# Optimization experiments

Measured on AMD Instinct MI355X. Metric: run time of the kernel, lower is better.

Reference implementation:

```python
import jax, jax.numpy as jnp
import numpy as np

B, T, C, H, N, FFN = 4, 1024, 2048, 32, 64, 7168
HEAD_DIVISOR = 8.0
EPS = 1e-5


def setup_inputs() -> dict:
    key = jax.random.key(0)
    ks = jax.random.split(key, 30)
    rn = lambda k, s, sc=0.02: jax.random.normal(k, s, jnp.float32) * sc
    ru = lambda k, s: jax.random.uniform(k, s, jnp.float32)
    return {
        "x": jax.random.normal(ks[0], (B, T, C), jnp.float32),
        "att_shift": jax.random.normal(ks[1], (B, C), jnp.float32),
        "wkv_state": jax.random.normal(ks[2], (B, H, N, N), jnp.float32) * 0.1,
        "ffn_shift": jax.random.normal(ks[3], (B, C), jnp.float32),
        "ln1_w": jnp.ones((C,), jnp.float32), "ln1_b": jnp.zeros((C,), jnp.float32),
        "ln2_w": jnp.ones((C,), jnp.float32), "ln2_b": jnp.zeros((C,), jnp.float32),
        "mix_k": ru(ks[4], (C,)), "mix_v": ru(ks[5], (C,)),
        "mix_r": ru(ks[6], (C,)), "mix_g": ru(ks[7], (C,)),
        "Wr": rn(ks[8], (C, C)), "Wk": rn(ks[9], (C, C)), "Wv": rn(ks[10], (C, C)),
        "Wg": rn(ks[11], (C, C)), "Wo": rn(ks[12], (C, C)),
        "time_decay": jax.random.normal(ks[13], (H, N), jnp.float32) * 0.5,
        "time_faaaa": jax.random.normal(ks[14], (H, N), jnp.float32) * 0.1,
        "gn_w": jnp.ones((C,), jnp.float32), "gn_b": jnp.zeros((C,), jnp.float32),
        "cmix_k": ru(ks[15], (C,)), "cmix_r": ru(ks[16], (C,)),
        "Wck": rn(ks[17], (C, FFN)), "Wcr": rn(ks[18], (C, C)), "Wcv": rn(ks[19], (FFN, C)),
    }


def _ln(z, w, b):
    m = z.mean(-1, keepdims=True)
    v = z.var(-1, keepdims=True)
    return (z - m) / jnp.sqrt(v + EPS) * w + b


def _shift(x, shift_state):
    # prepend carried last-token state, drop final position
    return jnp.concatenate([shift_state[:, None, :], x[:, :-1]], axis=1)


def reference(x, att_shift, wkv_state, ffn_shift, ln1_w, ln1_b, ln2_w, ln2_b,
              mix_k, mix_v, mix_r, mix_g, Wr, Wk, Wv, Wg, Wo,
              time_decay, time_faaaa, gn_w, gn_b, cmix_k, cmix_r, Wck, Wcr, Wcv):
    Bb, Tt, Cc = x.shape

    # ---- TimeMix ----
    x1 = _ln(x, ln1_w, ln1_b)
    xx = _shift(x1, att_shift)
    xk = x1 * mix_k + xx * (1 - mix_k)
    xv = x1 * mix_v + xx * (1 - mix_v)
    xr = x1 * mix_r + xx * (1 - mix_r)
    xg = x1 * mix_g + xx * (1 - mix_g)
    r = (xr @ Wr).reshape(Bb, Tt, H, N)
    k = (xk @ Wk).reshape(Bb, Tt, H, N)
    v = (xv @ Wv).reshape(Bb, Tt, H, N)
    g = jax.nn.silu(xg @ Wg)

    w = jnp.exp(-jnp.exp(time_decay))[None, :, :, None]  # [1,H,N,1] decay on k-index
    u = time_faaaa[None, :, :, None]                      # [1,H,N,1] bonus on current token

    def step(S, rkv):  # S: [B,H,N,N] (k-index i, v-index j)
        rr, kk, vv = rkv
        kv = kk[..., :, None] * vv[..., None, :]          # [B,H,N,N]
        y = jnp.einsum('bhi,bhij->bhj', rr, S + u * kv)
        return S * w + kv, y

    rkv = (jnp.moveaxis(r, 1, 0), jnp.moveaxis(k, 1, 0), jnp.moveaxis(v, 1, 0))
    new_wkv, ys = jax.lax.scan(step, wkv_state, rkv)      # ys: [T,B,H,N]
    att = jnp.moveaxis(ys, 0, 1)                          # [B,T,H,N]

    # GroupNorm(n_head groups) on att / head_size_divisor
    z = att / HEAD_DIVISOR
    m = z.mean(-1, keepdims=True)
    var = z.var(-1, keepdims=True)
    z = (z - m) / jnp.sqrt(var + EPS)
    z = z * gn_w.reshape(H, N) + gn_b.reshape(H, N)
    att_out = (z.reshape(Bb, Tt, Cc) * g) @ Wo

    x = x + att_out

    # ---- ChannelMix ----
    x2 = _ln(x, ln2_w, ln2_b)
    xx2 = _shift(x2, ffn_shift)
    xck = x2 * cmix_k + xx2 * (1 - cmix_k)
    xcr = x2 * cmix_r + xx2 * (1 - cmix_r)
    kk = jnp.square(jax.nn.relu(xck @ Wck))
    kv = kk @ Wcv
    ffn_out = jax.nn.sigmoid(xcr @ Wcr) * kv
    x = x + ffn_out

    return x, x1[:, -1], new_wkv, x2[:, -1]
```

## Files before the change

### kernel.cpp

```cpp
#include <hip/hip_runtime.h>
#include <cstdint>
#include <cstddef>

typedef unsigned short u16;
typedef unsigned int u32;
typedef short bf16x8 __attribute__((ext_vector_type(8)));
typedef unsigned short u16x4 __attribute__((ext_vector_type(4)));
typedef unsigned short u16x8 __attribute__((ext_vector_type(8)));
typedef float f32x4 __attribute__((ext_vector_type(4)));

#define DEV __device__ __forceinline__

constexpr int Bb = 4, Tt = 1024, Cc = 2048, Hh = 32, Nd = 64, FF = 7168;
constexpr int BT = Bb * Tt;
constexpr int NCH = 16;

DEV u16 f2bf(float f) {
  union { float f; unsigned u; } un; un.f = f;
  unsigned r = un.u + 0x7FFFu + ((un.u >> 16) & 1u);
  return (u16)(r >> 16);
}
DEV float bf2f(u16 h) {
  union { unsigned u; float f; } un; un.u = ((unsigned)h) << 16;
  return un.f;
}
DEV void gll16(const u16* gp, u16* lp) {
  __builtin_amdgcn_global_load_lds(
      (const __attribute__((address_space(1))) unsigned int*)gp,
      (__attribute__((address_space(3))) unsigned int*)lp,
      16, 0, 0);
}
DEV int xcd_swz(int f, int nwg) {
  int q = nwg >> 3;
  return (f & 7) * q + (f >> 3);
}

DEV void transp_body(const float* __restrict__ W, u16* __restrict__ Wt,
                     int Kk, int Nn, float (*tile)[33]) {
  int n0 = blockIdx.x * 32, k0 = blockIdx.y * 32;
  int tx = threadIdx.x & 31, ty = threadIdx.x >> 5;
  #pragma unroll
  for (int r = 0; r < 32; r += 8)
    tile[r + ty][tx] = W[(size_t)(k0 + r + ty) * Nn + n0 + tx];
  __syncthreads();
  #pragma unroll
  for (int r = 0; r < 32; r += 8)
    Wt[(size_t)(n0 + r + ty) * Kk + k0 + tx] = f2bf(tile[tx][r + ty]);
}

__global__ void transpose_to_bf16(const float* __restrict__ W, u16* __restrict__ Wt,
                                  int Kk, int Nn) {
  __shared__ float tile[32][33];
  transp_body(W, Wt, Kk, Nn, tile);
}

__global__ void transpose6_cc(const float* __restrict__ W0, const float* __restrict__ W1,
                              const float* __restrict__ W2, const float* __restrict__ W3,
                              const float* __restrict__ W4, const float* __restrict__ W5,
                              u16* __restrict__ T0, u16* __restrict__ T1,
                              u16* __restrict__ T2, u16* __restrict__ T3,
                              u16* __restrict__ T4, u16* __restrict__ T5) {
  __shared__ float tile[32][33];
  const int z = blockIdx.z;
  const float* W = (z == 0) ? W0 : (z == 1) ? W1 : (z == 2) ? W2 :
                   (z == 3) ? W3 : (z == 4) ? W4 : W5;
  u16* T = (z == 0) ? T0 : (z == 1) ? T1 : (z == 2) ? T2 :
           (z == 3) ? T3 : (z == 4) ? T4 : T5;
  transp_body(W, T, Cc, Cc, tile);
}

DEV void block_ln(const float* __restrict__ src, int tid, float* red,
                  float vals[8], float& mean, float& inv) {
  float s = 0.f, ss = 0.f;
  #pragma unroll
  for (int i = 0; i < 8; i++) {
    float t = src[tid + i * 256];
    vals[i] = t; s += t; ss += t * t;
  }
  #pragma unroll
  for (int m = 1; m < 64; m <<= 1) { s += __shfl_xor(s, m); ss += __shfl_xor(ss, m); }
  int lane = tid & 63, wv = tid >> 6;
  __syncthreads();
  if (lane == 0) { red[wv] = s; red[4 + wv] = ss; }
  __syncthreads();
  s = red[0] + red[1] + red[2] + red[3];
  ss = red[4] + red[5] + red[6] + red[7];
  mean = s * (1.f / Cc);
  float var = ss * (1.f / Cc) - mean * mean;
  inv = rsqrtf(var + 1e-5f);
}

__global__ __launch_bounds__(256)
void ln_mix4(const float* __restrict__ x, const float* __restrict__ shift,
             const float* __restrict__ w, const float* __restrict__ b,
             const float* __restrict__ mk, const float* __restrict__ mv,
             const float* __restrict__ mr, const float* __restrict__ mg,
             u16* __restrict__ xk, u16* __restrict__ xv,
             u16* __restrict__ xr, u16* __restrict__ xg,
             float* __restrict__ last) {
  int row = blockIdx.x;
  int t = row & (Tt - 1), bb = row >> 10;
  int tid = threadIdx.x;
  __shared__ float red[8];
  const float* cur = x + (size_t)row * Cc;
  float cv[8], pv[8], cm, ci, pm = 0.f, pi = 1.f;
  block_ln(cur, tid, red, cv, cm, ci);
  bool t0 = (t == 0);
  const float* prev = t0 ? (shift + (size_t)bb * Cc) : (cur - Cc);
  if (!t0) {
    block_ln(prev, tid, red, pv, pm, pi);
  } else {
    #pragma unroll
    for (int i = 0; i < 8; i++) pv[i] = prev[tid + i * 256];
  }
  size_t o = (size_t)row * Cc;
  bool isLast = (t == Tt - 1);
  #pragma unroll
  for (int i = 0; i < 8; i++) {
    int c = tid + i * 256;
    float xc = (cv[i] - cm) * ci * w[c] + b[c];
    float xp = t0 ? pv[i] : (pv[i] - pm) * pi * w[c] + b[c];
    xk[o + c] = f2bf(xp + mk[c] * (xc - xp));
    xv[o + c] = f2bf(xp + mv[c] * (xc - xp));
    xr[o + c] = f2bf(xp + mr[c] * (xc - xp));
    xg[o + c] = f2bf(xp + mg[c] * (xc - xp));
    if (isLast) last[(size_t)bb * Cc + c] = xc;
  }
}

__global__ __launch_bounds__(256)
void ln_mix2(const float* __restrict__ x, const float* __restrict__ shift,
             const float* __restrict__ w, const float* __restrict__ b,
             const float* __restrict__ ck, const float* __restrict__ cr,
             u16* __restrict__ xck, u16* __restrict__ xcr,
             float* __restrict__ last) {
  int row = blockIdx.x;
  int t = row & (Tt - 1), bb = row >> 10;
  int tid = threadIdx.x;
  __shared__ float red[8];
  const float* cur = x + (size_t)row * Cc;
  float cv[8], pv[8], cm, ci, pm = 0.f, pi = 1.f;
  block_ln(cur, tid, red, cv, cm, ci);
  bool t0 = (t == 0);
  const float* prev = t0 ? (shift + (size_t)bb * Cc) : (cur - Cc);
  if (!t0) {
    block_ln(prev, tid, red, pv, pm, pi);
  } else {
    #pragma unroll
    for (int i = 0; i < 8; i++) pv[i] = prev[tid + i * 256];
  }
  size_t o = (size_t)row * Cc;
  bool isLast = (t == Tt - 1);
  #pragma unroll
  for (int i = 0; i < 8; i++) {
    int c = tid + i * 256;
    float xc = (cv[i] - cm) * ci * w[c] + b[c];
    float xp = t0 ? pv[i] : (pv[i] - pm) * pi * w[c] + b[c];
    xck[o + c] = f2bf(xp + ck[c] * (xc - xp));
    xcr[o + c] = f2bf(xp + cr[c] * (xc - xp));
    if (isLast) last[(size_t)bb * Cc + c] = xc;
  }
}

DEV int swzoff(int row, int off) {
  return (row << 7) +
         (off ^ ((((row >> 1) & 1) << 4) | (((row >> 2) & 1) << 5) | (((row >> 3) & 1) << 6)));
}

DEV void stage_half(const u16* __restrict__ gbase, int ldK, u16* slot, int tid) {
  #pragma unroll
  for (int c2 = 0; c2 < 2; c2++) {
    const int D = c2 * 8192 + tid * 16;
    const int row = D >> 7;
    const int off = (D & 127) ^ ((((row >> 1) & 1) << 4) | (((row >> 2) & 1) << 5) | (((row >> 3) & 1) << 6));
    gll16(gbase + (size_t)row * ldK + (off >> 1), (u16*)((char*)slot + D));
  }
}

template <int EPI, int NB>
DEV void g256_core(const u16* __restrict__ A, const u16* __restrict__ Bt,
                   int N, int K, int ldK,
                   float* __restrict__ Co, u16* __restrict__ Cb,
                   const float* __restrict__ X1, const float* __restrict__ X2,
                   const u16* __restrict__ X2b,
                   u16 (*lds)[8192], int m0, int n0, int act) {
  const int tid = threadIdx.x;
  const int w = tid >> 6, lane = tid & 63;
  const int l15 = lane & 15, l4 = lane >> 4;
  const int wm = (w & 3) * 64;
  const int wn = (w >> 2) * (NB * 64);
  const int ahalf = wm >> 7;
  const int arow0 = wm & 127;
  const int bhalf = (NB == 2) ? (w >> 2) : 0;
  const int nt = K >> 6;

  const u16* Ag = A + (size_t)m0 * ldK;
  const u16* Bg = Bt + (size_t)n0 * ldK;

  f32x4 acc[4][NB * 4] = {};
  bf16x8 a[4][2];

  stage_half(Ag, ldK, lds[0], tid);
  stage_half(Ag + (size_t)128 * ldK, ldK, lds[1], tid);
  stage_half(Bg, ldK, lds[4], tid);
  if constexpr (NB == 2) stage_half(Bg + (size_t)128 * ldK, ldK, lds[5], tid);
  if (nt > 1) {
    stage_half(Ag + 64, ldK, lds[2], tid);
    stage_half(Ag + (size_t)128 * ldK + 64, ldK, lds[3], tid);
    asm volatile("s_waitcnt vmcnt(4)" ::: "memory");
  } else {
    asm volatile("s_waitcnt vmcnt(0)" ::: "memory");
  }
  asm volatile("s_barrier" ::: "memory");

  for (int t = 0; t < nt; t++) {
    const int buf = t & 1;
    const char* Aslot = (const char*)lds[buf * 2 + ahalf];
    const char* Bslot = (const char*)lds[4 + buf * NB + bhalf];

#define G256_PHASE(p)                                                                       \
    {                                                                                       \
      constexpr int nh = (p) >> 1, kh = (p) & 1;                                            \
      if constexpr ((p) < 2) {                                                              \
        _Pragma("unroll")                                                                   \
        for (int mf = 0; mf < 4; mf++) {                                                    \
          const int row = arow0 + mf * 16 + l15;                                            \
          a[mf][kh] = *(const bf16x8*)(Aslot + swzoff(row, kh * 64 + l4 * 16));             \
        }                                                                                   \
      }                                                                                     \
      bf16x8 bfr[2 * NB];                                                                   \
      _Pragma("unroll")                                                                     \
      for (int j = 0; j < 2 * NB; j++) {                                                    \
        const int row = (NB == 2 ? 0 : wn) + (nh * 2 * NB + j) * 16 + l15;                  \
        bfr[j] = *(const bf16x8*)(Bslot + swzoff(row, kh * 64 + l4 * 16));                  \
      }                                                                                     \
      if constexpr ((p) == 0) {                                                             \
        if (t + 1 < nt) stage_half(Bg + (size_t)(t + 1) * 64, ldK,                          \
                                   lds[4 + ((t + 1) & 1) * NB], tid);                       \
      } else if constexpr ((p) == 1) {                                                      \
        if constexpr (NB == 2) {                                                            \
          if (t + 1 < nt) stage_half(Bg + (size_t)128 * ldK + (size_t)(t + 1) * 64, ldK,    \
                                     lds[4 + ((t + 1) & 1) * NB + 1], tid);                 \
        }                                                                                   \
      } else if constexpr ((p) == 2) {                                                      \
        if (t + 2 < nt) stage_half(Ag + (size_t)(t + 2) * 64, ldK, lds[buf << 1], tid);     \
      } else {                                                                              \
        if (t + 2 < nt) stage_half(Ag + (size_t)128 * ldK + (size_t)(t + 2) * 64, ldK,      \
                                   lds[(buf << 1) + 1], tid);                               \
      }                                                                                     \
      asm volatile("s_barrier" ::: "memory");                                               \
      __builtin_amdgcn_s_setprio(1);                                                       \
      _Pragma("unroll")                                                                     \
      for (int mf = 0; mf < 4; mf++)                                                        \
        _Pragma("unroll")                                                                   \
        for (int j = 0; j < 2 * NB; j++)                                                    \
          acc[mf][nh * 2 * NB + j] = __builtin_amdgcn_mfma_f32_16x16x32_bf16(               \
              a[mf][kh], bfr[j], acc[mf][nh * 2 * NB + j], 0, 0, 0);                        \
      __builtin_amdgcn_s_setprio(0);                                                       \
      if constexpr ((p) == 3) {                                                             \
        if (t + 2 < nt) asm volatile("s_waitcnt vmcnt(4)" ::: "memory");                    \
        else            asm volatile("s_waitcnt vmcnt(0)" ::: "memory");                    \
      }                                                                                     \
      asm volatile("s_barrier" ::: "memory");                                               \
    }

    G256_PHASE(0)
    G256_PHASE(1)
    G256_PHASE(2)
    G256_PHASE(3)
#undef G256_PHASE
  }

  #pragma unroll
  for (int mf = 0; mf < 4; mf++) {
    #pragma unroll
    for (int reg = 0; reg < 4; reg++) {
      const int gr = m0 + wm + mf * 16 + l4 * 4 + reg;
      const size_t ro = (size_t)gr * N;
      #pragma unroll
      for (int nf = 0; nf < NB * 4; nf++) {
        const int gc = n0 + wn + nf * 16 + l15;
        float val = acc[mf][nf][reg];
        if constexpr (EPI == 0) {
          Co[ro + gc] = val;
        } else if constexpr (EPI == 1) {
          if (act) val = val / (1.f + __expf(-val));
          Cb[ro + gc] = f2bf(val);
        } else if constexpr (EPI == 3) {
          float tr = fmaxf(val, 0.f);
          Cb[ro + gc] = f2bf(tr * tr);
        } else if constexpr (EPI == 4) {
          Co[ro + gc] = X1[ro + gc] + val;
        } else {
          float s = 1.f / (1.f + __expf(-val));
          float kvv = X2[ro + gc] + bf2f(X2b[ro + gc]);
          Co[ro + gc] = fmaf(s, kvv, X1[ro + gc]);
        }
      }
    }
  }
}

template <int EPI>
__global__ __launch_bounds__(512)
void gemm256s(const u16* __restrict__ A, const u16* __restrict__ Bt,
              int N, int K,
              float* __restrict__ Co, u16* __restrict__ Cb,
              const float* __restrict__ X1, int NX) {
  __shared__ __align__(16) u16 lds[8][8192];
  int o = xcd_swz(blockIdx.x, gridDim.x);
  int xb = o % NX, yb = o / NX;
  g256_core<EPI, 2>(A, Bt, N, K, K, Co, Cb, X1, nullptr, nullptr, lds,
                    yb * 256, xb * 256, 0);
}

template <int EPI>
__global__ __launch_bounds__(512)
void gemm128s(const u16* __restrict__ A, const u16* __restrict__ Bt,
              int N, int K,
              float* __restrict__ Co, u16* __restrict__ Cb,
              const float* __restrict__ X1, const float* __restrict__ X2,
              const u16* __restrict__ X2b, int NX) {
  __shared__ __align__(16) u16 lds[6][8192];
  int o = xcd_swz(blockIdx.x, gridDim.x);
  int xb = o % NX, yb = o / NX;
  g256_core<EPI, 1>(A, Bt, N, K, K, Co, Cb, X1, X2, X2b, lds,
                    yb * 256, xb * 128, 0);
}

__global__ __launch_bounds__(512)
void gemm256_proj(const u16* __restrict__ A0, const u16* __restrict__ A1,
                  const u16* __restrict__ A2, const u16* __restrict__ A3,
                  const u16* __restrict__ B0, const u16* __restrict__ B1,
                  const u16* __restrict__ B2, const u16* __restrict__ B3,
                  u16* __restrict__ C0, u16* __restrict__ C1,
                  u16* __restrict__ C2, u16* __restrict__ C3) {
  __shared__ __align__(16) u16 lds[8][8192];
  int o = xcd_swz(blockIdx.x, gridDim.x);
  int xb = o & 7, yb = (o >> 3) & 15, z = o >> 7;
  const u16* A = (z == 0) ? A0 : (z == 1) ? A1 : (z == 2) ? A2 : A3;
  const u16* Bt = (z == 0) ? B0 : (z == 1) ? B1 : (z == 2) ? B2 : B3;
  u16* Cb = (z == 0) ? C0 : (z == 1) ? C1 : (z == 2) ? C2 : C3;
  g256_core<1, 2>(A, Bt, Cc, Cc, Cc, nullptr, Cb, nullptr, nullptr, nullptr, lds,
                  yb * 256, xb * 256, z == 3);
}

__global__ __launch_bounds__(512)
void gemm256_splitk(const u16* __restrict__ A, const u16* __restrict__ Bt,
                    float* __restrict__ kv0, u16* __restrict__ kv1) {
  __shared__ __align__(16) u16 lds[8][8192];
  int o = xcd_swz(blockIdx.x, gridDim.x);
  int xb = o & 7, yb = (o >> 3) & 15, z = o >> 7;
  const int Koff = z * (FF / 2);
  if (z == 0)
    g256_core<0, 2>(A + Koff, Bt + Koff, Cc, FF / 2, FF, kv0, nullptr,
                    nullptr, nullptr, nullptr, lds, yb * 256, xb * 256, 0);
  else
    g256_core<1, 2>(A + Koff, Bt + Koff, Cc, FF / 2, FF, nullptr, kv1,
                    nullptr, nullptr, nullptr, lds, yb * 256, xb * 256, 0);
}

__global__ __launch_bounds__(256)
void wkv_pre(const u16* __restrict__ rg, const u16* __restrict__ kg,
             const u16* __restrict__ vg, const float* __restrict__ td,
             const float* __restrict__ tf,
             float* __restrict__ Yb, float* __restrict__ Db,
             u16* __restrict__ Rtb) {
  __shared__ float Pt[64][68];
  __shared__ float uL[64];
  __shared__ u16 rB[64 * 72];
  __shared__ u16 kB[64 * 72];
  __shared__ u16 Rh[64 * 72];
  __shared__ u16 KhX[96 * 72];
  __shared__ u16 vA[64 * 72];
  __shared__ u16 Vt[64 * 72];

  const int tid = threadIdx.x, bid = blockIdx.x;
  const int bh = bid >> 4, c = bid & 15;
  const int b = bh >> 5, h = bh & 31;
  const int lane = tid & 63, w = tid >> 6;

  {
    int i = tid & 63;
    float d = __expf(td[h * 64 + i]);
    float c1 = -1.4426950408889634f * d;
    int e0 = (tid >> 6) * 16;
    #pragma unroll
    for (int e = 0; e < 16; e++) Pt[e0 + e][i] = exp2f(c1 * (float)(e0 + e));
    if (tid < 64) uL[tid] = tf[h * 64 + tid];
  }
  __syncthreads();

  const int row = tid >> 2, col0 = (tid & 3) * 16;
  const int tl = row & 15;
  {
    size_t gro = ((size_t)b * Tt + c * 64 + row) * Cc + h * 64 + col0;
    u16x8 rv0 = *(const u16x8*)(rg + gro);
    u16x8 rv1 = *(const u16x8*)(rg + gro + 8);
    u16x8 kv0 = *(const u16x8*)(kg + gro);
    u16x8 kv1 = *(const u16x8*)(kg + gro + 8);
    u16x8 vv0 = *(const u16x8*)(vg + gro);
    u16x8 vv1 = *(const u16x8*)(vg + gro + 8);
    *(u16x8*)&rB[row * 72 + col0] = rv0; *(u16x8*)&rB[row * 72 + col0 + 8] = rv1;
    *(u16x8*)&kB[row * 72 + col0] = kv0; *(u16x8*)&kB[row * 72 + col0 + 8] = kv1;
    *(u16x8*)&vA[row * 72 + col0] = vv0; *(u16x8*)&vA[row * 72 + col0 + 8] = vv1;
    float rf[16], kf[16];
    #pragma unroll
    for (int e = 0; e < 8; e++) { rf[e] = bf2f(rv0[e]); rf[8 + e] = bf2f(rv1[e]); }
    #pragma unroll
    for (int e = 0; e < 8; e++) { kf[e] = bf2f(kv0[e]); kf[8 + e] = bf2f(kv1[e]); }
    u16x8 o0, o1, t0_, t1_;
    #pragma unroll
    for (int e = 0; e < 8; e++) {
      o0[e] = f2bf(rf[e] * Pt[tl][col0 + e]);
      o1[e] = f2bf(rf[8 + e] * Pt[tl][col0 + 8 + e]);
      t0_[e] = f2bf(rf[e] * Pt[row][col0 + e]);
      t1_[e] = f2bf(rf[8 + e] * Pt[row][col0 + 8 + e]);
    }
    *(u16x8*)&Rh[row * 72 + col0] = o0; *(u16x8*)&Rh[row * 72 + col0 + 8] = o1;
    u16* rtp = Rtb + (size_t)bid * 4096 + row * 64 + col0;
    *(u16x8*)rtp = t0_; *(u16x8*)(rtp + 8) = t1_;
    if (row < 48) {
      u16x8 a0, a1;
      #pragma unroll
      for (int e = 0; e < 8; e++) {
        a0[e] = f2bf(kf[e] * Pt[15 - tl][col0 + e]);
        a1[e] = f2bf(kf[8 + e] * Pt[15 - tl][col0 + 8 + e]);
      }
      *(u16x8*)&KhX[row * 72 + col0] = a0; *(u16x8*)&KhX[row * 72 + col0 + 8] = a1;
    }
    if (row < 32) {
      u16x8 a0, a1;
      #pragma unroll
      for (int e = 0; e < 8; e++) {
        a0[e] = f2bf(kf[e] * Pt[31 - tl][col0 + e]);
        a1[e] = f2bf(kf[8 + e] * Pt[31 - tl][col0 + 8 + e]);
      }
      *(u16x8*)&KhX[(48 + row) * 72 + col0] = a0; *(u16x8*)&KhX[(48 + row) * 72 + col0 + 8] = a1;
    }
    if (row < 16) {
      u16x8 a0, a1;
      #pragma unroll
      for (int e = 0; e < 8; e++) {
        a0[e] = f2bf(kf[e] * Pt[47 - tl][col0 + e]);
        a1[e] = f2bf(kf[8 + e] * Pt[47 - tl][col0 + 8 + e]);
      }
      *(u16x8*)&KhX[(80 + row) * 72 + col0] = a0; *(u16x8*)&KhX[(80 + row) * 72 + col0 + 8] = a1;
    }
  }
  __syncthreads();

  {
    const int jj = tid & 63, s0 = (tid >> 6) * 16;
    #pragma unroll
    for (int ds = 0; ds < 16; ds += 2) {
      u32 pk = ((u32)vA[(s0 + ds + 1) * 72 + jj] << 16) | vA[(s0 + ds) * 72 + jj];
      *(u32*)&Vt[jj * 72 + s0 + ds] = pk;
    }
  }
  __syncthreads();

  u16* aB = vA;
  {
    const int pr[6] = {1, 2, 3, 2, 3, 3};
    const int qr[6] = {0, 1, 2, 0, 1, 0};
    const int dr[6] = {0, 0, 0, 1, 1, 2};
    const int lr = lane & 15, kq = lane >> 4;
    for (int pi = w; pi < 6; pi += 4) {
      const int p = pr[pi], q = qr[pi], d = dr[pi];
      const int kbase = (d == 0) ? q * 16 : (d == 1) ? 48 + q * 16 : 80 + q * 16;
      f32x4 aacc = {};
      #pragma unroll
      for (int kf2 = 0; kf2 < 2; kf2++) {
        bf16x8 af = *(const bf16x8*)&Rh[(p * 16 + lr) * 72 + kf2 * 32 + kq * 8];
        bf16x8 bf_ = *(const bf16x8*)&KhX[(kbase + lr) * 72 + kf2 * 32 + kq * 8];
        aacc = __builtin_amdgcn_mfma_f32_16x16x32_bf16(af, bf_, aacc, 0, 0, 0);
      }
      #pragma unroll
      for (int reg = 0; reg < 4; reg++) {
        aB[(p * 16 + kq * 4 + reg) * 72 + q * 16 + lr] = f2bf(aacc[reg]);
        aB[(q * 16 + kq * 4 + reg) * 72 + p * 16 + lr] = 0;
      }
    }
    for (int e = lane; e < 256; e += 64) {
      const int tl2 = e >> 4, sl = e & 15;
      float a = 0.f;
      if (sl <= tl2) {
        const u16* rp = &rB[(w * 16 + tl2) * 72];
        const u16* kp = &kB[(w * 16 + sl) * 72];
        const float* pp = (sl == tl2) ? uL : &Pt[tl2 - 1 - sl][0];
        #pragma unroll
        for (int i0 = 0; i0 < 64; i0 += 4) {
          u16x4 ra = *(const u16x4*)(rp + i0);
          u16x4 ka = *(const u16x4*)(kp + i0);
          f32x4 pa = *(const f32x4*)(pp + i0);
          #pragma unroll
          for (int di = 0; di < 4; di++)
            a = fmaf(bf2f(ra[di]) * bf2f(ka[di]), pa[di], a);
        }
      }
      aB[(w * 16 + tl2) * 72 + w * 16 + sl] = f2bf(a);
    }
  }
  __syncthreads();

  u16* Ktt = KhX;
  {
    const int ii = tid & 63, s0 = (tid >> 6) * 16;
    #pragma unroll
    for (int ds = 0; ds < 16; ds += 2) {
      float v0 = bf2f(kB[(s0 + ds) * 72 + ii]) * Pt[63 - (s0 + ds)][ii];
      float v1 = bf2f(kB[(s0 + ds + 1) * 72 + ii]) * Pt[63 - (s0 + ds + 1)][ii];
      u32 pk = ((u32)f2bf(v1) << 16) | f2bf(v0);
      *(u32*)&Ktt[ii * 72 + s0 + ds] = pk;
    }
  }
  __syncthreads();

  const int lr = lane & 15, kq = lane >> 4;
  {
    f32x4 yac[4] = {};
    #pragma unroll
    for (int kf2 = 0; kf2 < 2; kf2++) {
      bf16x8 af = *(const bf16x8*)&aB[(w * 16 + lr) * 72 + kf2 * 32 + kq * 8];
      #pragma unroll
      for (int nf = 0; nf < 4; nf++) {
        bf16x8 bf_ = *(const bf16x8*)&Vt[(nf * 16 + lr) * 72 + kf2 * 32 + kq * 8];
        yac[nf] = __builtin_amdgcn_mfma_f32_16x16x32_bf16(af, bf_, yac[nf], 0, 0, 0);
      }
    }
    float* Yp = Yb + (size_t)bid * 4096;
    #pragma unroll
    for (int nf = 0; nf < 4; nf++)
      #pragma unroll
      for (int reg = 0; reg < 4; reg++)
        Yp[(w * 16 + kq * 4 + reg) * 64 + nf * 16 + lr] = yac[nf][reg];

    f32x4 dac[4] = {};
    #pragma unroll
    for (int kf2 = 0; kf2 < 2; kf2++) {
      bf16x8 af = *(const bf16x8*)&Ktt[(w * 16 + lr) * 72 + kf2 * 32 + kq * 8];
      #pragma unroll
      for (int nf = 0; nf < 4; nf++) {
        bf16x8 bf_ = *(const bf16x8*)&Vt[(nf * 16 + lr) * 72 + kf2 * 32 + kq * 8];
        dac[nf] = __builtin_amdgcn_mfma_f32_16x16x32_bf16(af, bf_, dac[nf], 0, 0, 0);
      }
    }
    float* Dp = Db + (size_t)bid * 4096;
    #pragma unroll
    for (int nf = 0; nf < 4; nf++)
      #pragma unroll
      for (int reg = 0; reg < 4; reg++)
        Dp[(w * 16 + kq * 4 + reg) * 64 + nf * 16 + lr] = dac[nf][reg];
  }
}

__global__ __launch_bounds__(256)
void wkv_scan(const float* __restrict__ s0g, const float* __restrict__ td,
              const float* __restrict__ Db, u16* __restrict__ Sbb,
              float* __restrict__ sout) {
  const int bh = blockIdx.x, h = bh & 31;
  const int tid = threadIdx.x;
  const int i = tid >> 2, j0 = (tid & 3) * 16;
  float d = __expf(td[h * 64 + i]);
  float w64 = exp2f(-1.4426950408889634f * d * 64.f);
  f32x4 S[4];
  const float* sp = s0g + ((size_t)bh * 64 + i) * 64 + j0;
  #pragma unroll
  for (int q = 0; q < 4; q++) S[q] = *(const f32x4*)(sp + q * 4);
  for (int c = 0; c < NCH; c++) {
    u16* op = Sbb + ((size_t)(bh * 16 + c)) * 4096 + i * 64 + j0;
    u16x8 o0, o1;
    #pragma unroll
    for (int e = 0; e < 4; e++) { o0[e] = f2bf(S[0][e]); o0[4 + e] = f2bf(S[1][e]);
                                  o1[e] = f2bf(S[2][e]); o1[4 + e] = f2bf(S[3][e]); }
    *(u16x8*)op = o0; *(u16x8*)(op + 8) = o1;
    const float* dp = Db + ((size_t)(bh * 16 + c)) * 4096 + i * 64 + j0;
    #pragma unroll
    for (int q = 0; q < 4; q++) {
      f32x4 dv = *(const f32x4*)(dp + q * 4);
      #pragma unroll
      for (int e = 0; e < 4; e++) S[q][e] = fmaf(w64, S[q][e], dv[e]);
    }
  }
  float* fo = sout + ((size_t)bh * 64 + i) * 64 + j0;
  #pragma unroll
  for (int q = 0; q < 4; q++) *(f32x4*)(fo + q * 4) = S[q];
}

__global__ __launch_bounds__(256)
void wkv_post(const u16* __restrict__ Rtb, const u16* __restrict__ Sbb,
              const float* __restrict__ Yb, const u16* __restrict__ g,
              const float* __restrict__ gnw, const float* __restrict__ gnb,
              u16* __restrict__ xo) {
  __shared__ u16 Rt[64 * 72];
  __shared__ u16 St[64 * 72];
  __shared__ u16 xoL[64 * 72];
  const int tid = threadIdx.x, bid = blockIdx.x;
  const int bh = bid >> 4, c = bid & 15;
  const int b = bh >> 5, h = bh & 31;
  const int lane = tid & 63, w = tid >> 6;
  const int row = tid >> 2, col0 = (tid & 3) * 16;

  {
    const u16* rp = Rtb + (size_t)bid * 4096 + row * 64 + col0;
    u16x8 a0 = *(const u16x8*)rp, a1 = *(const u16x8*)(rp + 8);
    *(u16x8*)&Rt[row * 72 + col0] = a0; *(u16x8*)&Rt[row * 72 + col0 + 8] = a1;
  }
  {
    const u16* sp = Sbb + ((size_t)(bh * 16 + c)) * 4096 + row * 64 + col0;
    u16x8 s0 = *(const u16x8*)sp, s1 = *(const u16x8*)(sp + 8);
    #pragma unroll
    for (int e = 0; e < 8; e++) {
      St[(col0 + e) * 72 + row] = s0[e];
      St[(col0 + 8 + e) * 72 + row] = s1[e];
    }
  }
  const int lr = lane & 15, kq = lane >> 4;
  f32x4 acc[4];
  {
    const float* Yp = Yb + (size_t)bid * 4096;
    #pragma unroll
    for (int nf = 0; nf < 4; nf++)
      #pragma unroll
      for (int reg = 0; reg < 4; reg++)
        acc[nf][reg] = Yp[(w * 16 + kq * 4 + reg) * 64 + nf * 16 + lr];
  }
  __syncthreads();
  #pragma unroll
  for (int kf2 = 0; kf2 < 2; kf2++) {
    bf16x8 af = *(const bf16x8*)&Rt[(w * 16 + lr) * 72 + kf2 * 32 + kq * 8];
    #pragma unroll
    for (int nf = 0; nf < 4; nf++) {
      bf16x8 bf_ = *(const bf16x8*)&St[(nf * 16 + lr) * 72 + kf2 * 32 + kq * 8];
      acc[nf] = __builtin_amdgcn_mfma_f32_16x16x32_bf16(af, bf_, acc[nf], 0, 0, 0);
    }
  }
  #pragma unroll
  for (int reg = 0; reg < 4; reg++) {
    float s = 0.f, ss = 0.f;
    #pragma unroll
    for (int nf = 0; nf < 4; nf++) {
      float z = acc[nf][reg] * 0.125f;
      s += z; ss += z * z;
    }
    #pragma unroll
    for (int m = 1; m < 16; m <<= 1) { s += __shfl_xor(s, m); ss += __shfl_xor(ss, m); }
    float mean = s * (1.f / 64.f);
    float var = ss * (1.f / 64.f) - mean * mean;
    float inv = rsqrtf(var + 1e-5f);
    const int tau = w * 16 + kq * 4 + reg;
    #pragma unroll
    for (int nf = 0; nf < 4; nf++) {
      const int col = nf * 16 + lr;
      float z = acc[nf][reg] * 0.125f;
      float zn = (z - mean) * inv * gnw[h * 64 + col] + gnb[h * 64 + col];
      float gv = bf2f(g[((size_t)b * Tt + c * 64 + tau) * Cc + h * 64 + col]);
      xoL[tau * 72 + col] = f2bf(zn * gv);
    }
  }
  __syncthreads();
  {
    u16x8 o0 = *(const u16x8*)&xoL[row * 72 + col0];
    u16x8 o1 = *(const u16x8*)&xoL[row * 72 + col0 + 8];
    u16* xop = xo + ((size_t)b * Tt + c * 64 + row) * Cc + h * 64 + col0;
    *(u16x8*)xop = o0; *(u16x8*)(xop + 8) = o1;
  }
}

extern "C" void kernel_launch(void* const* d_in, const int* in_sizes, int n_in,
                              void* d_out, int out_size, void* d_ws, size_t ws_size,
                              hipStream_t stream) {
  const float* x         = (const float*)d_in[0];
  const float* att_shift = (const float*)d_in[1];
  const float* wkv0      = (const float*)d_in[2];
  const float* ffn_shift = (const float*)d_in[3];
  const float* ln1w = (const float*)d_in[4];
  const float* ln1b = (const float*)d_in[5];
  const float* ln2w = (const float*)d_in[6];
  const float* ln2b = (const float*)d_in[7];
  const float* mixk = (const float*)d_in[8];
  const float* mixv = (const float*)d_in[9];
  const float* mixr = (const float*)d_in[10];
  const float* mixg = (const float*)d_in[11];
  const float* Wr = (const float*)d_in[12];
  const float* Wk = (const float*)d_in[13];
  const float* Wv = (const float*)d_in[14];
  const float* Wg = (const float*)d_in[15];
  const float* Wo = (const float*)d_in[16];
  const float* td = (const float*)d_in[17];
  const float* tf = (const float*)d_in[18];
  const float* gnw = (const float*)d_in[19];
  const float* gnb = (const float*)d_in[20];
  const float* cmk = (const float*)d_in[21];
  const float* cmr = (const float*)d_in[22];
  const float* Wck = (const float*)d_in[23];
  const float* Wcr = (const float*)d_in[24];
  const float* Wcv = (const float*)d_in[25];

  constexpr size_t SZ_CC = (size_t)Cc * Cc * 2;
  constexpr size_t SZ_CF = (size_t)Cc * FF * 2;
  constexpr size_t SZ_AB = (size_t)BT * Cc * 2;
  constexpr size_t O_W   = 0;
  constexpr size_t O_R1  = 6 * SZ_CC + 2 * SZ_CF;
  constexpr size_t R1_SZ = 4 * SZ_AB;
  constexpr size_t O_R2  = O_R1 + R1_SZ;
  constexpr size_t R2_SZ = 3 * SZ_AB;
  constexpr size_t O_R3  = O_R2 + R2_SZ;
  constexpr size_t WS_NEED = O_R3 + SZ_AB;

  if (ws_size < WS_NEED) return;

  char* ws = (char*)d_ws;
  u16* WrT  = (u16*)(ws + O_W);
  u16* WkT  = (u16*)(ws + O_W + 1 * SZ_CC);
  u16* WvT  = (u16*)(ws + O_W + 2 * SZ_CC);
  u16* WgT  = (u16*)(ws + O_W + 3 * SZ_CC);
  u16* WoT  = (u16*)(ws + O_W + 4 * SZ_CC);
  u16* WcrT = (u16*)(ws + O_W + 5 * SZ_CC);
  u16* WckT = (u16*)(ws + O_W + 6 * SZ_CC);
  u16* WcvT = (u16*)(ws + O_W + 6 * SZ_CC + SZ_CF);

  u16*   xk  = (u16*)(ws + O_R1);
  u16*   xv  = (u16*)(ws + O_R1 + SZ_AB);
  u16*   xr  = (u16*)(ws + O_R1 + 2 * SZ_AB);
  u16*   xg  = (u16*)(ws + O_R1 + 3 * SZ_AB);
  float* Yb  = (float*)(ws + O_R1);
  u16*   Rtb = (u16*)(ws + O_R1 + 2 * SZ_AB);
  u16*   Sbb = (u16*)(ws + O_R1 + 3 * SZ_AB);
  u16*   kk  = (u16*)(ws + O_R1);
  u16*   rb  = (u16*)(ws + O_R2);
  u16*   kb  = (u16*)(ws + O_R2 + SZ_AB);
  u16*   vb  = (u16*)(ws + O_R2 + 2 * SZ_AB);
  u16*   xcr = (u16*)(ws + O_R2);
  u16*   xck = (u16*)(ws + O_R2 + SZ_AB);
  u16*   xo  = (u16*)(ws + O_R2 + 2 * SZ_AB);
  float* kv0 = (float*)(ws + O_R2 + SZ_AB);
  u16*   gbuf = (u16*)(ws + O_R3);
  u16*   kv1  = (u16*)(ws + O_R3);

  float* out      = (float*)d_out;
  float* x1_last  = out + (size_t)BT * Cc;
  float* wkv_out  = x1_last + (size_t)Bb * Cc;
  float* x2_last  = wkv_out + (size_t)Bb * Hh * Nd * Nd;
  float* Db       = out;

  transpose6_cc<<<dim3(64, 64, 6), 256, 0, stream>>>(Wr, Wk, Wv, Wg, Wo, Wcr,
                                                     WrT, WkT, WvT, WgT, WoT, WcrT);
  transpose_to_bf16<<<dim3(224, 64), 256, 0, stream>>>(Wck, WckT, Cc, FF);
  transpose_to_bf16<<<dim3(64, 224), 256, 0, stream>>>(Wcv, WcvT, FF, Cc);

  ln_mix4<<<BT, 256, 0, stream>>>(x, att_shift, ln1w, ln1b,
                                  mixk, mixv, mixr, mixg, xk, xv, xr, xg, x1_last);
  gemm256_proj<<<512, 512, 0, stream>>>(xr, xk, xv, xg,
                                        WrT, WkT, WvT, WgT,
                                        rb, kb, vb, gbuf);
  wkv_pre<<<Bb * Hh * NCH, 256, 0, stream>>>(rb, kb, vb, td, tf, Yb, Db, Rtb);
  wkv_scan<<<Bb * Hh, 256, 0, stream>>>(wkv0, td, Db, Sbb, wkv_out);
  wkv_post<<<Bb * Hh * NCH, 256, 0, stream>>>(Rtb, Sbb, Yb, gbuf, gnw, gnb, xo);
  gemm128s<4><<<256, 512, 0, stream>>>(xo, WoT, Cc, Cc, out, nullptr, x,
                                       nullptr, nullptr, 16);
  ln_mix2<<<BT, 256, 0, stream>>>(out, ffn_shift, ln2w, ln2b, cmk, cmr, xck, xcr, x2_last);
  gemm256s<3><<<448, 512, 0, stream>>>(xck, WckT, FF, Cc, nullptr, kk, nullptr, 28);
  gemm256_splitk<<<256, 512, 0, stream>>>(kk, WcvT, kv0, kv1);
  gemm128s<6><<<256, 512, 0, stream>>>(xcr, WcrT, Cc, Cc, out, nullptr, out,
                                       kv0, kv1, 16);

  (void)in_sizes; (void)n_in; (void)out_size;
}
```

Before: 724.5 us.

## Switch 256-tile GEMM core to 32x32x16 MFMA and vectorize weight transposes

The shared 256-wide GEMM core moves from 16x16x32 bf16 MFMA to 32x32x16 MFMA. Its k-loop is restructured into two half-phases per K tile, with A fragments loaded once per tile and the epilogue row/column mapping rewritten for the 32x32 accumulator layout. The aim is fewer LDS fragment reads per FLOP and fewer MFMA issues. Separately, the fp32-to-bf16 weight transposes drop the LDS tile and instead use 4x4 register transposes with float4 loads and 8-byte stores. The transposes trade some coalescing on the strided bf16 writes for less LDS traffic and synchronization.

```diff
diff --git a/kernel.cpp b/kernel.cpp
--- a/kernel.cpp
+++ b/kernel.cpp
@@ -8,6 +8,7 @@
 typedef unsigned short u16x4 __attribute__((ext_vector_type(4)));
 typedef unsigned short u16x8 __attribute__((ext_vector_type(8)));
 typedef float f32x4 __attribute__((ext_vector_type(4)));
+typedef float f32x16 __attribute__((ext_vector_type(16)));
 
 #define DEV __device__ __forceinline__
 
@@ -35,38 +36,41 @@
   return (f & 7) * q + (f >> 3);
 }
 
-DEV void transp_body(const float* __restrict__ W, u16* __restrict__ Wt,
-                     int Kk, int Nn, float (*tile)[33]) {
-  int n0 = blockIdx.x * 32, k0 = blockIdx.y * 32;
-  int tx = threadIdx.x & 31, ty = threadIdx.x >> 5;
-  #pragma unroll
-  for (int r = 0; r < 32; r += 8)
-    tile[r + ty][tx] = W[(size_t)(k0 + r + ty) * Nn + n0 + tx];
-  __syncthreads();
-  #pragma unroll
-  for (int r = 0; r < 32; r += 8)
-    Wt[(size_t)(n0 + r + ty) * Kk + k0 + tx] = f2bf(tile[tx][r + ty]);
-}
-
-__global__ void transpose_to_bf16(const float* __restrict__ W, u16* __restrict__ Wt,
-                                  int Kk, int Nn) {
-  __shared__ float tile[32][33];
-  transp_body(W, Wt, Kk, Nn, tile);
-}
-
-__global__ void transpose6_cc(const float* __restrict__ W0, const float* __restrict__ W1,
-                              const float* __restrict__ W2, const float* __restrict__ W3,
-                              const float* __restrict__ W4, const float* __restrict__ W5,
-                              u16* __restrict__ T0, u16* __restrict__ T1,
-                              u16* __restrict__ T2, u16* __restrict__ T3,
-                              u16* __restrict__ T4, u16* __restrict__ T5) {
-  __shared__ float tile[32][33];
+DEV void transp64_body(const float* __restrict__ W, u16* __restrict__ Wt,
+                       int Kk, int Nn) {
+  const int n0 = blockIdx.x * 64, k0 = blockIdx.y * 64;
+  const int tx = threadIdx.x & 15, ty = threadIdx.x >> 4;
+  const int kk = k0 + ty * 4, nn = n0 + tx * 4;
+  const float* p = W + (size_t)kk * Nn + nn;
+  f32x4 r0 = *(const f32x4*)(p);
+  f32x4 r1 = *(const f32x4*)(p + (size_t)Nn);
+  f32x4 r2 = *(const f32x4*)(p + 2 * (size_t)Nn);
+  f32x4 r3 = *(const f32x4*)(p + 3 * (size_t)Nn);
+  #pragma unroll
+  for (int j = 0; j < 4; j++) {
+    u16x4 o;
+    o[0] = f2bf(r0[j]); o[1] = f2bf(r1[j]); o[2] = f2bf(r2[j]); o[3] = f2bf(r3[j]);
+    *(u16x4*)(Wt + (size_t)(nn + j) * Kk + kk) = o;
+  }
+}
+
+__global__ void transp64(const float* __restrict__ W, u16* __restrict__ Wt,
+                         int Kk, int Nn) {
+  transp64_body(W, Wt, Kk, Nn);
+}
+
+__global__ void transp64_6cc(const float* __restrict__ W0, const float* __restrict__ W1,
+                             const float* __restrict__ W2, const float* __restrict__ W3,
+                             const float* __restrict__ W4, const float* __restrict__ W5,
+                             u16* __restrict__ T0, u16* __restrict__ T1,
+                             u16* __restrict__ T2, u16* __restrict__ T3,
+                             u16* __restrict__ T4, u16* __restrict__ T5) {
   const int z = blockIdx.z;
   const float* W = (z == 0) ? W0 : (z == 1) ? W1 : (z == 2) ? W2 :
                    (z == 3) ? W3 : (z == 4) ? W4 : W5;
   u16* T = (z == 0) ? T0 : (z == 1) ? T1 : (z == 2) ? T2 :
            (z == 3) ? T3 : (z == 4) ? T4 : T5;
-  transp_body(W, T, Cc, Cc, tile);
+  transp64_body(W, T, Cc, Cc);
 }
 
 DEV void block_ln(const float* __restrict__ src, int tid, float* red,
@@ -186,7 +190,7 @@
                    u16 (*lds)[8192], int m0, int n0, int act) {
   const int tid = threadIdx.x;
   const int w = tid >> 6, lane = tid & 63;
-  const int l15 = lane & 15, l4 = lane >> 4;
+  const int l31 = lane & 31, l5 = lane >> 5;
   const int wm = (w & 3) * 64;
   const int wn = (w >> 2) * (NB * 64);
   const int ahalf = wm >> 7;
@@ -197,8 +201,8 @@
   const u16* Ag = A + (size_t)m0 * ldK;
   const u16* Bg = Bt + (size_t)n0 * ldK;
 
-  f32x4 acc[4][NB * 4] = {};
-  bf16x8 a[4][2];
+  f32x16 acc[2][2 * NB] = {};
+  bf16x8 a[2][4];
 
   stage_half(Ag, ldK, lds[0], tid);
   stage_half(Ag + (size_t)128 * ldK, ldK, lds[1], tid);
@@ -218,68 +222,77 @@
     const char* Aslot = (const char*)lds[buf * 2 + ahalf];
     const char* Bslot = (const char*)lds[4 + buf * NB + bhalf];
 
-#define G256_PHASE(p)                                                                       \
-    {                                                                                       \
-      constexpr int nh = (p) >> 1, kh = (p) & 1;                                            \
-      if constexpr ((p) < 2) {                                                              \
-        _Pragma("unroll")                                                                   \
-        for (int mf = 0; mf < 4; mf++) {                                                    \
-          const int row = arow0 + mf * 16 + l15;                                            \
-          a[mf][kh] = *(const bf16x8*)(Aslot + swzoff(row, kh * 64 + l4 * 16));             \
-        }                                                                                   \
-      }                                                                                     \
-      bf16x8 bfr[2 * NB];                                                                   \
-      _Pragma("unroll")                                                                     \
-      for (int j = 0; j < 2 * NB; j++) {                                                    \
-        const int row = (NB == 2 ? 0 : wn) + (nh * 2 * NB + j) * 16 + l15;                  \
-        bfr[j] = *(const bf16x8*)(Bslot + swzoff(row, kh * 64 + l4 * 16));                  \
-      }                                                                                     \
-      if constexpr ((p) == 0) {                                                             \
-        if (t + 1 < nt) stage_half(Bg + (size_t)(t + 1) * 64, ldK,                          \
-                                   lds[4 + ((t + 1) & 1) * NB], tid);                       \
-      } else if constexpr ((p) == 1) {                                                      \
-        if constexpr (NB == 2) {                                                            \
-          if (t + 1 < nt) stage_half(Bg + (size_t)128 * ldK + (size_t)(t + 1) * 64, ldK,    \
-                                     lds[4 + ((t + 1) & 1) * NB + 1], tid);                 \
-        }                                                                                   \
-      } else if constexpr ((p) == 2) {                                                      \
-        if (t + 2 < nt) stage_half(Ag + (size_t)(t + 2) * 64, ldK, lds[buf << 1], tid);     \
-      } else {                                                                              \
-        if (t + 2 < nt) stage_half(Ag + (size_t)128 * ldK + (size_t)(t + 2) * 64, ldK,      \
-                                   lds[(buf << 1) + 1], tid);                               \
-      }                                                                                     \
-      asm volatile("s_barrier" ::: "memory");                                               \
-      __builtin_amdgcn_s_setprio(1);                                                       \
-      _Pragma("unroll")                                                                     \
-      for (int mf = 0; mf < 4; mf++)                                                        \
-        _Pragma("unroll")                                                                   \
-        for (int j = 0; j < 2 * NB; j++)                                                    \
-          acc[mf][nh * 2 * NB + j] = __builtin_amdgcn_mfma_f32_16x16x32_bf16(               \
-              a[mf][kh], bfr[j], acc[mf][nh * 2 * NB + j], 0, 0, 0);                        \
-      __builtin_amdgcn_s_setprio(0);                                                       \
-      if constexpr ((p) == 3) {                                                             \
-        if (t + 2 < nt) asm volatile("s_waitcnt vmcnt(4)" ::: "memory");                    \
-        else            asm volatile("s_waitcnt vmcnt(0)" ::: "memory");                    \
-      }                                                                                     \
-      asm volatile("s_barrier" ::: "memory");                                               \
-    }
-
-    G256_PHASE(0)
-    G256_PHASE(1)
-    G256_PHASE(2)
-    G256_PHASE(3)
-#undef G256_PHASE
-  }
-
-  #pragma unroll
-  for (int mf = 0; mf < 4; mf++) {
-    #pragma unroll
-    for (int reg = 0; reg < 4; reg++) {
-      const int gr = m0 + wm + mf * 16 + l4 * 4 + reg;
+    #pragma unroll
+    for (int mf = 0; mf < 2; mf++)
+      #pragma unroll
+      for (int ks = 0; ks < 4; ks++)
+        a[mf][ks] = *(const bf16x8*)(Aslot + swzoff(arow0 + mf * 32 + l31, ks * 32 + l5 * 16));
+    {
+      bf16x8 b[NB][4];
+      #pragma unroll
+      for (int nf = 0; nf < NB; nf++)
+        #pragma unroll
+        for (int ks = 0; ks < 4; ks++)
+          b[nf][ks] = *(const bf16x8*)(Bslot +
+              swzoff((NB == 2 ? 0 : wn) + nf * 32 + l31, ks * 32 + l5 * 16));
+      if (t + 1 < nt) {
+        stage_half(Bg + (size_t)(t + 1) * 64, ldK, lds[4 + ((t + 1) & 1) * NB], tid);
+        if constexpr (NB == 2)
+          stage_half(Bg + (size_t)128 * ldK + (size_t)(t + 1) * 64, ldK,
+                     lds[4 + ((t + 1) & 1) * NB + 1], tid);
+      }
+      asm volatile("s_barrier" ::: "memory");
+      __builtin_amdgcn_s_setprio(1);
+      #pragma unroll
+      for (int mf = 0; mf < 2; mf++)
+        #pragma unroll
+        for (int nf = 0; nf < NB; nf++)
+          #pragma unroll
+          for (int ks = 0; ks < 4; ks++)
+            acc[mf][nf] = __builtin_amdgcn_mfma_f32_32x32x16_bf16(
+                a[mf][ks], b[nf][ks], acc[mf][nf], 0, 0, 0);
+      __builtin_amdgcn_s_setprio(0);
+      asm volatile("s_barrier" ::: "memory");
+    }
+    {
+      bf16x8 b[NB][4];
+      #pragma unroll
+      for (int nf = 0; nf < NB; nf++)
+        #pragma unroll
+        for (int ks = 0; ks < 4; ks++)
+          b[nf][ks] = *(const bf16x8*)(Bslot +
+              swzoff((NB == 2 ? 0 : wn) + (NB + nf) * 32 + l31, ks * 32 + l5 * 16));
+      if (t + 2 < nt) {
+        stage_half(Ag + (size_t)(t + 2) * 64, ldK, lds[buf << 1], tid);
+        stage_half(Ag + (size_t)128 * ldK + (size_t)(t + 2) * 64, ldK,
+                   lds[(buf << 1) + 1], tid);
+      }
+      asm volatile("s_barrier" ::: "memory");
+      __builtin_amdgcn_s_setprio(1);
+      #pragma unroll
+      for (int mf = 0; mf < 2; mf++)
+        #pragma unroll
+        for (int nf = 0; nf < NB; nf++)
+          #pragma unroll
+          for (int ks = 0; ks < 4; ks++)
+            acc[mf][NB + nf] = __builtin_amdgcn_mfma_f32_32x32x16_bf16(
+                a[mf][ks], b[nf][ks], acc[mf][NB + nf], 0, 0, 0);
+      __builtin_amdgcn_s_setprio(0);
+      if (t + 2 < nt) asm volatile("s_waitcnt vmcnt(4)" ::: "memory");
+      else            asm volatile("s_waitcnt vmcnt(0)" ::: "memory");
+      asm volatile("s_barrier" ::: "memory");
+    }
+  }
+
+  #pragma unroll
+  for (int mf = 0; mf < 2; mf++) {
+    #pragma unroll
+    for (int reg = 0; reg < 16; reg++) {
+      const int gr = m0 + wm + mf * 32 + (reg & 3) + 8 * (reg >> 2) + 4 * l5;
       const size_t ro = (size_t)gr * N;
       #pragma unroll
-      for (int nf = 0; nf < NB * 4; nf++) {
-        const int gc = n0 + wn + nf * 16 + l15;
+      for (int nf = 0; nf < 2 * NB; nf++) {
+        const int gc = n0 + wn + nf * 32 + l31;
         float val = acc[mf][nf][reg];
         if constexpr (EPI == 0) {
           Co[ro + gc] = val;
@@ -745,10 +758,10 @@
   float* x2_last  = wkv_out + (size_t)Bb * Hh * Nd * Nd;
   float* Db       = out;
 
-  transpose6_cc<<<dim3(64, 64, 6), 256, 0, stream>>>(Wr, Wk, Wv, Wg, Wo, Wcr,
-                                                     WrT, WkT, WvT, WgT, WoT, WcrT);
-  transpose_to_bf16<<<dim3(224, 64), 256, 0, stream>>>(Wck, WckT, Cc, FF);
-  transpose_to_bf16<<<dim3(64, 224), 256, 0, stream>>>(Wcv, WcvT, FF, Cc);
+  transp64_6cc<<<dim3(32, 32, 6), 256, 0, stream>>>(Wr, Wk, Wv, Wg, Wo, Wcr,
+                                                    WrT, WkT, WvT, WgT, WoT, WcrT);
+  transp64<<<dim3(112, 32), 256, 0, stream>>>(Wck, WckT, Cc, FF);
+  transp64<<<dim3(32, 112), 256, 0, stream>>>(Wcv, WcvT, FF, Cc);
 
   ln_mix4<<<BT, 256, 0, stream>>>(x, att_shift, ln1w, ln1b,
                                   mixk, mixv, mixr, mixg, xk, xv, xr, xg, x1_last);
```

New measurement: 750.7 us. 3.6% more time.
